# Kernel tuning notes

Hardware: AMD Instinct MI355X
Metric: run time of the kernel (lower is better)

## Reference

```python
import jax, jax.numpy as jnp
from jax import lax
import numpy as np

B, S, IN, H, L = 32, 512, 512, 1024, 4


def setup_inputs() -> dict:
    key = jax.random.key(0)
    ks = jax.random.split(key, 6)
    scale = 0.02
    return {
        "x": jax.random.normal(ks[0], (B, S, IN), jnp.float32),
        "w_ih0": jax.random.normal(ks[1], (3 * H, IN), jnp.float32) * scale,
        "w_hh0": jax.random.normal(ks[2], (3 * H, H), jnp.float32) * scale,
        "b0": jnp.zeros((3 * H,), jnp.float32),
        "w_ih_rest": jax.random.normal(ks[3], (L - 1, 3 * H, H), jnp.float32) * scale,
        "w_hh_rest": jax.random.normal(ks[4], (L - 1, 3 * H, H), jnp.float32) * scale,
        "b_rest": jnp.zeros((L - 1, 3 * H), jnp.float32),
    }


def _run_layer(xs, w_ih, w_hh, b):
    # xs: [B, S, D_in] -> outputs [B, S, H], final (h, c) each [B, H]
    batch = xs.shape[0]
    hid = w_hh.shape[1]

    def step(carry, x_t):
        h, c = carry
        gates = x_t @ w_ih.T + h @ w_hh.T + b  # [B, 3H]
        i_g, g_g, o_g = jnp.split(gates, 3, axis=1)
        c_next = c + jax.nn.sigmoid(i_g) * jnp.tanh(g_g)  # no forget gate (CEC)
        h_next = jax.nn.sigmoid(o_g) * jnp.tanh(c_next)
        return (h_next, c_next), h_next

    init = (jnp.zeros((batch, hid), xs.dtype), jnp.zeros((batch, hid), xs.dtype))
    (h_f, c_f), ys = lax.scan(step, init, jnp.swapaxes(xs, 0, 1))  # scan over time
    return jnp.swapaxes(ys, 0, 1), h_f, c_f


def reference(x, w_ih0, w_hh0, b0, w_ih_rest, w_hh_rest, b_rest):
    h_finals, c_finals = [], []
    cur, h_f, c_f = _run_layer(x, w_ih0, w_hh0, b0)
    h_finals.append(h_f)
    c_finals.append(c_f)
    for i in range(w_ih_rest.shape[0]):
        cur, h_f, c_f = _run_layer(cur, w_ih_rest[i], w_hh_rest[i], b_rest[i])
        h_finals.append(h_f)
        c_finals.append(c_f)
    return cur, (jnp.stack(h_finals), jnp.stack(c_finals))
```

## Files before the change

### kernel.cpp

```cpp
#include <hip/hip_runtime.h>


typedef unsigned short ushort_t;
typedef __attribute__((ext_vector_type(4))) float f32x4;
typedef __attribute__((ext_vector_type(8))) short s16x8;
typedef __attribute__((ext_vector_type(4))) short s16x4;

__device__ __forceinline__ unsigned short f2bf(float f) {
  union { float f; unsigned u; } v; v.f = f;
  unsigned r = (v.u + 0x7fffu + ((v.u >> 16) & 1u)) >> 16;
  return (unsigned short)r;
}
__device__ __forceinline__ float bf2f(unsigned short h) {
  union { unsigned u; float f; } v; v.u = ((unsigned)h) << 16; return v.f;
}
__device__ __forceinline__ void split2(float x, short& hi, short& lo) {
  unsigned short h = f2bf(x);
  hi = (short)h;
  lo = (short)f2bf(x - bf2f(h));
}

#define BM 128
#define BN 128
#define BK 32
__global__ __launch_bounds__(256) void k_gemm_split(
    const float* __restrict__ A, const float* __restrict__ Bw,
    const float* __restrict__ bias, float* __restrict__ C,
    int M, int N, int K) {
  __shared__ short Ah[BM * BK], Al[BM * BK];
  __shared__ short Bh[BN * BK], Bl[BN * BK];
  const int tid = threadIdx.x;
  const int nbm = M / BM;
  const int bm = blockIdx.x % nbm;
  const int bn = blockIdx.x / nbm;
  const int lane = tid & 63;
  const int wave = tid >> 6;
  const int wm = (wave & 1) * 64;
  const int wn = (wave >> 1) * 64;
  const int q = lane >> 4;
  f32x4 acc[4][4] = {};
  const int nk = K / BK;
  for (int kt = 0; kt < nk; ++kt) {
    __syncthreads();
    const int kb = kt * BK;
#pragma unroll
    for (int i = 0; i < 4; ++i) {
      int idx = tid + i * 256;
      int row = idx >> 3, c4 = (idx & 7) * 4;
      f32x4 ta = *(const f32x4*)(A + (size_t)(bm * BM + row) * K + kb + c4);
      s16x4 h4, l4;
#pragma unroll
      for (int j = 0; j < 4; ++j) { short hh, ll; split2(ta[j], hh, ll); h4[j] = hh; l4[j] = ll; }
      *(s16x4*)&Ah[row * BK + c4] = h4;
      *(s16x4*)&Al[row * BK + c4] = l4;
      f32x4 tb = *(const f32x4*)(Bw + (size_t)(bn * BN + row) * K + kb + c4);
#pragma unroll
      for (int j = 0; j < 4; ++j) { short hh, ll; split2(tb[j], hh, ll); h4[j] = hh; l4[j] = ll; }
      *(s16x4*)&Bh[row * BK + c4] = h4;
      *(s16x4*)&Bl[row * BK + c4] = l4;
    }
    __syncthreads();
    s16x8 ah[4], al[4], bh[4], bl[4];
#pragma unroll
    for (int i = 0; i < 4; ++i) {
      int r = (wm + i * 16 + (lane & 15)) * BK + q * 8;
      ah[i] = *(const s16x8*)&Ah[r];
      al[i] = *(const s16x8*)&Al[r];
      int rb = (wn + i * 16 + (lane & 15)) * BK + q * 8;
      bh[i] = *(const s16x8*)&Bh[rb];
      bl[i] = *(const s16x8*)&Bl[rb];
    }
#pragma unroll
    for (int mi = 0; mi < 4; ++mi)
#pragma unroll
      for (int ni = 0; ni < 4; ++ni) {
        acc[mi][ni] = __builtin_amdgcn_mfma_f32_16x16x32_bf16(ah[mi], bh[ni], acc[mi][ni], 0, 0, 0);
        acc[mi][ni] = __builtin_amdgcn_mfma_f32_16x16x32_bf16(al[mi], bh[ni], acc[mi][ni], 0, 0, 0);
        acc[mi][ni] = __builtin_amdgcn_mfma_f32_16x16x32_bf16(ah[mi], bl[ni], acc[mi][ni], 0, 0, 0);
      }
  }
#pragma unroll
  for (int mi = 0; mi < 4; ++mi)
#pragma unroll
    for (int ni = 0; ni < 4; ++ni) {
      int col = bn * BN + wn + ni * 16 + (lane & 15);
      float bv = bias[col];
#pragma unroll
      for (int r = 0; r < 4; ++r) {
        int row = bm * BM + wm + mi * 16 + q * 4 + r;
        C[(size_t)row * N + col] = acc[mi][ni][r] + bv;
      }
    }
}

__global__ __launch_bounds__(128) void k_recurrent(
    const float* __restrict__ Xp,
    const float* __restrict__ Whh,
    unsigned* __restrict__ hbuf,
    float* __restrict__ yOut,
    float* __restrict__ hOut,
    float* __restrict__ cOut,
    int* __restrict__ bar)
{
  __shared__ short Wh[128 * 12 * 8];
  __shared__ short Wl[128 * 12 * 8];
  __shared__ float red[2][16][16];
  const int tid = threadIdx.x;
  const int lane = tid & 63;
  const int g = tid >> 6;
  const int bid = blockIdx.x;
  const int s = ((bid & 7) << 5) | (bid >> 3);
  const int u0 = s * 4;
  const int b0 = g * 16;

  for (int p = tid; p < 1536; p += 128) {
    int n = p >> 7, kq = p & 127;
    int row = (n < 4) ? (u0 + n) : (n < 8) ? (1024 + u0 + (n - 4)) : (2048 + u0 + (n - 8));
    const float* src = Whh + (size_t)row * 1024 + kq * 8;
    f32x4 v0 = *(const f32x4*)src;
    f32x4 v1 = *(const f32x4*)(src + 4);
    s16x4 h4, l4;
#pragma unroll
    for (int j = 0; j < 4; ++j) { short hh, ll; split2(v0[j], hh, ll); h4[j] = hh; l4[j] = ll; }
    *(s16x4*)&Wh[(kq * 12 + n) * 8] = h4;
    *(s16x4*)&Wl[(kq * 12 + n) * 8] = l4;
#pragma unroll
    for (int j = 0; j < 4; ++j) { short hh, ll; split2(v1[j], hh, ll); h4[j] = hh; l4[j] = ll; }
    *(s16x4*)&Wh[(kq * 12 + n) * 8 + 4] = h4;
    *(s16x4*)&Wl[(kq * 12 + n) * 8 + 4] = l4;
  }

  const int m = lane & 15;
  const int q = lane >> 4;
  const bool nvalid = m < 12;
  const int eb = (tid >> 2) & 15;
  const int eu = tid & 3;
  const int kc0 = s & 31;
  float c = 0.f;
  __syncthreads();

  for (int t = 0; t < 512; ++t) {
    const int par = t & 1;
    const size_t mrow = (size_t)(b0 + eb) * 512 + t;
    const float xi = Xp[mrow * 3072 + (u0 + eu)];
    const float xg = Xp[mrow * 3072 + 1024 + (u0 + eu)];
    const float xo = Xp[mrow * 3072 + 2048 + (u0 + eu)];

    const unsigned* hp = hbuf + (size_t)par * 32768 + (b0 + m);
    f32x4 a0 = {0.f, 0.f, 0.f, 0.f}, a1 = a0, a2 = a0;
#pragma unroll 16
    for (int kci = 0; kci < 32; ++kci) {
      const int kc = (kci + kc0) & 31;
      const unsigned* p = hp + (kc * 32 + q * 8) * 32;
      unsigned w0 = __hip_atomic_load(p + 0 * 32, __ATOMIC_RELAXED, __HIP_MEMORY_SCOPE_AGENT);
      unsigned w1 = __hip_atomic_load(p + 1 * 32, __ATOMIC_RELAXED, __HIP_MEMORY_SCOPE_AGENT);
      unsigned w2 = __hip_atomic_load(p + 2 * 32, __ATOMIC_RELAXED, __HIP_MEMORY_SCOPE_AGENT);
      unsigned w3 = __hip_atomic_load(p + 3 * 32, __ATOMIC_RELAXED, __HIP_MEMORY_SCOPE_AGENT);
      unsigned w4 = __hip_atomic_load(p + 4 * 32, __ATOMIC_RELAXED, __HIP_MEMORY_SCOPE_AGENT);
      unsigned w5 = __hip_atomic_load(p + 5 * 32, __ATOMIC_RELAXED, __HIP_MEMORY_SCOPE_AGENT);
      unsigned w6 = __hip_atomic_load(p + 6 * 32, __ATOMIC_RELAXED, __HIP_MEMORY_SCOPE_AGENT);
      unsigned w7 = __hip_atomic_load(p + 7 * 32, __ATOMIC_RELAXED, __HIP_MEMORY_SCOPE_AGENT);
      union { unsigned u[4]; s16x8 v; } H, L;
      H.u[0] = (w0 >> 16) | (w1 & 0xffff0000u); L.u[0] = (w0 & 0xffffu) | (w1 << 16);
      H.u[1] = (w2 >> 16) | (w3 & 0xffff0000u); L.u[1] = (w2 & 0xffffu) | (w3 << 16);
      H.u[2] = (w4 >> 16) | (w5 & 0xffff0000u); L.u[2] = (w4 & 0xffffu) | (w5 << 16);
      H.u[3] = (w6 >> 16) | (w7 & 0xffff0000u); L.u[3] = (w6 & 0xffffu) | (w7 << 16);
      s16x8 ahf = H.v, alf = L.v;
      s16x8 bhf = {}, blf = {};
      if (nvalid) {
        bhf = *(const s16x8*)&Wh[(((kc * 4 + q) * 12) + m) * 8];
        blf = *(const s16x8*)&Wl[(((kc * 4 + q) * 12) + m) * 8];
      }
      a0 = __builtin_amdgcn_mfma_f32_16x16x32_bf16(ahf, bhf, a0, 0, 0, 0);
      a1 = __builtin_amdgcn_mfma_f32_16x16x32_bf16(alf, bhf, a1, 0, 0, 0);
      a2 = __builtin_amdgcn_mfma_f32_16x16x32_bf16(ahf, blf, a2, 0, 0, 0);
    }
#pragma unroll
    for (int r = 0; r < 4; ++r)
      red[g][q * 4 + r][m] = a0[r] + a1[r] + a2[r];
    __syncthreads();

    {
      float ig = xi + red[g][eb][eu];
      float gg = xg + red[g][eb][4 + eu];
      float og = xo + red[g][eb][8 + eu];
      float si = 1.f / (1.f + expf(-ig));
      float tg = tanhf(gg);
      c += si * tg;
      float so = 1.f / (1.f + expf(-og));
      float h = so * tanhf(c);
      short hh, hl;
      split2(h, hh, hl);
      unsigned hword = ((unsigned)(unsigned short)hh << 16) | (unsigned)(unsigned short)hl;
      size_t hw = (size_t)(1 - par) * 32768 + (size_t)(u0 + eu) * 32 + (b0 + eb);
      __hip_atomic_store(&hbuf[hw], hword, __ATOMIC_RELAXED, __HIP_MEMORY_SCOPE_AGENT);
      yOut[mrow * 1024 + (u0 + eu)] = h;
      if (t == 511) {
        hOut[(size_t)(b0 + eb) * 1024 + (u0 + eu)] = h;
        cOut[(size_t)(b0 + eb) * 1024 + (u0 + eu)] = c;
      }
    }
    if (t == 511) break;

    const int tgt = t + 1;
    asm volatile("s_waitcnt vmcnt(0)" ::: "memory");
    __syncthreads();
    if (bid == 0) {
      if (tid == 0)
        __hip_atomic_store(&bar[0], tgt, __ATOMIC_RELAXED, __HIP_MEMORY_SCOPE_AGENT);
      for (;;) {
        int f0 = __hip_atomic_load(&bar[tid], __ATOMIC_RELAXED, __HIP_MEMORY_SCOPE_AGENT);
        int f1 = __hip_atomic_load(&bar[tid + 128], __ATOMIC_RELAXED, __HIP_MEMORY_SCOPE_AGENT);
        if (__syncthreads_and((f0 >= tgt) && (f1 >= tgt))) break;
        __builtin_amdgcn_s_sleep(1);
      }
      if (tid == 0)
        __hip_atomic_store(&bar[256], tgt, __ATOMIC_RELAXED, __HIP_MEMORY_SCOPE_AGENT);
    } else {
      if (tid == 0) {
        __hip_atomic_store(&bar[bid], tgt, __ATOMIC_RELAXED, __HIP_MEMORY_SCOPE_AGENT);
        while (__hip_atomic_load(&bar[256], __ATOMIC_RELAXED, __HIP_MEMORY_SCOPE_AGENT) < tgt)
          __builtin_amdgcn_s_sleep(1);
      }
      __syncthreads();
    }
    asm volatile("" ::: "memory");
  }
}

extern "C" void kernel_launch(void* const* d_in, const int* in_sizes, int n_in,
                              void* d_out, int out_size, void* d_ws, size_t ws_size,
                              hipStream_t stream) {
  const float* x     = (const float*)d_in[0];
  const float* w_ih0 = (const float*)d_in[1];
  const float* w_hh0 = (const float*)d_in[2];
  const float* b0v   = (const float*)d_in[3];
  const float* w_ihr = (const float*)d_in[4];
  const float* w_hhr = (const float*)d_in[5];
  const float* b_r   = (const float*)d_in[6];
  float* out = (float*)d_out;

  char* ws = (char*)d_ws;
  float*    Xp   = (float*)(ws);
  unsigned* hbuf = (unsigned*)(ws + 201326592);
  int*      bar  = (int*)(ws + 201588736);

  float* yBuf     = out;
  float* hOutBase = out + 16777216;
  float* cOutBase = out + 16777216 + 131072;

  hipMemsetAsync(bar, 0, 8192, stream);

  for (int l = 0; l < 4; ++l) {
    const float* wih  = (l == 0) ? w_ih0 : (w_ihr + (size_t)(l - 1) * 3072 * 1024);
    const float* whh  = (l == 0) ? w_hh0 : (w_hhr + (size_t)(l - 1) * 3072 * 1024);
    const float* bias = (l == 0) ? b0v : (b_r + (size_t)(l - 1) * 3072);
    const int K = (l == 0) ? 512 : 1024;
    const float* Ain = (l == 0) ? x : yBuf;
    dim3 ggrid((16384 / BM) * (3072 / BN));
    k_gemm_split<<<ggrid, 256, 0, stream>>>(Ain, wih, bias, Xp, 16384, 3072, K);
    hipMemsetAsync(hbuf, 0, 262144, stream);
    float* hO = hOutBase + (size_t)l * 32768;
    float* cO = cOutBase + (size_t)l * 32768;
    int* barL = bar + l * 512;
    void* args[] = { (void*)&Xp, (void*)&whh, (void*)&hbuf, (void*)&yBuf,
                     (void*)&hO, (void*)&cO, (void*)&barL };
    if (hipLaunchCooperativeKernel((void*)k_recurrent, dim3(256), dim3(128),
                                   args, 0, stream) != hipSuccess) {
      k_recurrent<<<dim3(256), dim3(128), 0, stream>>>(Xp, whh, hbuf, yBuf,
                                                       hO, cO, barL);
    }
  }
}
```

Baseline: 19.13 ms.

## Remap recurrent blocks to one wave covering 8 units and 16 batches

The persistent recurrent kernel now uses a single 64-thread wave per block. Each block owns 8 hidden units (24 weight rows) for one 16-row batch group, where before a 128-thread block covered 4 units across two batch groups. Each wave issues twice as many MFMAs per h-fragment load, which halves the redundant hbuf reads per block and the per-unit LDS weight traffic. In exchange each block does twice the per-step serial MFMA work and the grid barrier handles four flags per thread.

```diff
diff --git a/kernel.cpp b/kernel.cpp
--- a/kernel.cpp
+++ b/kernel.cpp
@@ -93,7 +93,7 @@
     }
 }
 
-__global__ __launch_bounds__(128) void k_recurrent(
+__global__ __launch_bounds__(64) void k_recurrent(
     const float* __restrict__ Xp,
     const float* __restrict__ Whh,
     unsigned* __restrict__ hbuf,
@@ -102,53 +102,54 @@
     float* __restrict__ cOut,
     int* __restrict__ bar)
 {
-  __shared__ short Wh[128 * 12 * 8];
-  __shared__ short Wl[128 * 12 * 8];
-  __shared__ float red[2][16][16];
+  __shared__ short Wh[128 * 25 * 8];
+  __shared__ short Wl[128 * 25 * 8];
+  __shared__ float red[16][28];
   const int tid = threadIdx.x;
-  const int lane = tid & 63;
-  const int g = tid >> 6;
   const int bid = blockIdx.x;
-  const int s = ((bid & 7) << 5) | (bid >> 3);
-  const int u0 = s * 4;
-  const int b0 = g * 16;
-
-  for (int p = tid; p < 1536; p += 128) {
+  const int slice = ((bid & 7) << 4) | ((bid >> 3) & 15);
+  const int grp = bid >> 7;
+  const int u0 = slice * 8;
+  const int b0 = grp * 16;
+
+  for (int p = tid; p < 3072; p += 64) {
     int n = p >> 7, kq = p & 127;
-    int row = (n < 4) ? (u0 + n) : (n < 8) ? (1024 + u0 + (n - 4)) : (2048 + u0 + (n - 8));
+    int r = (n > 11) ? 1 : 0, rr = n - r * 12, G = rr >> 2, ui = rr & 3;
+    int row = G * 1024 + u0 + r * 4 + ui;
     const float* src = Whh + (size_t)row * 1024 + kq * 8;
     f32x4 v0 = *(const f32x4*)src;
     f32x4 v1 = *(const f32x4*)(src + 4);
     s16x4 h4, l4;
 #pragma unroll
     for (int j = 0; j < 4; ++j) { short hh, ll; split2(v0[j], hh, ll); h4[j] = hh; l4[j] = ll; }
-    *(s16x4*)&Wh[(kq * 12 + n) * 8] = h4;
-    *(s16x4*)&Wl[(kq * 12 + n) * 8] = l4;
+    *(s16x4*)&Wh[(kq * 25 + n) * 8] = h4;
+    *(s16x4*)&Wl[(kq * 25 + n) * 8] = l4;
 #pragma unroll
     for (int j = 0; j < 4; ++j) { short hh, ll; split2(v1[j], hh, ll); h4[j] = hh; l4[j] = ll; }
-    *(s16x4*)&Wh[(kq * 12 + n) * 8 + 4] = h4;
-    *(s16x4*)&Wl[(kq * 12 + n) * 8 + 4] = l4;
-  }
-
-  const int m = lane & 15;
-  const int q = lane >> 4;
+    *(s16x4*)&Wh[(kq * 25 + n) * 8 + 4] = h4;
+    *(s16x4*)&Wl[(kq * 25 + n) * 8 + 4] = l4;
+  }
+
+  const int m = tid & 15;
+  const int q = tid >> 4;
   const bool nvalid = m < 12;
-  const int eb = (tid >> 2) & 15;
-  const int eu = tid & 3;
-  const int kc0 = s & 31;
-  float c = 0.f;
+  const int kc0 = slice & 31;
+  float cA = 0.f, cB = 0.f;
   __syncthreads();
 
   for (int t = 0; t < 512; ++t) {
     const int par = t & 1;
-    const size_t mrow = (size_t)(b0 + eb) * 512 + t;
-    const float xi = Xp[mrow * 3072 + (u0 + eu)];
-    const float xg = Xp[mrow * 3072 + 1024 + (u0 + eu)];
-    const float xo = Xp[mrow * 3072 + 2048 + (u0 + eu)];
+    const size_t mrow = (size_t)(b0 + m) * 512 + t;
+    const float xiA = Xp[mrow * 3072 + (u0 + q)];
+    const float xiB = Xp[mrow * 3072 + (u0 + q + 4)];
+    const float xgA = Xp[mrow * 3072 + 1024 + (u0 + q)];
+    const float xgB = Xp[mrow * 3072 + 1024 + (u0 + q + 4)];
+    const float xoA = Xp[mrow * 3072 + 2048 + (u0 + q)];
+    const float xoB = Xp[mrow * 3072 + 2048 + (u0 + q + 4)];
 
     const unsigned* hp = hbuf + (size_t)par * 32768 + (b0 + m);
-    f32x4 a0 = {0.f, 0.f, 0.f, 0.f}, a1 = a0, a2 = a0;
-#pragma unroll 16
+    f32x4 acc[2][3] = {};
+#pragma unroll 8
     for (int kci = 0; kci < 32; ++kci) {
       const int kc = (kci + kc0) & 31;
       const unsigned* p = hp + (kc * 32 + q * 8) * 32;
@@ -166,38 +167,54 @@
       H.u[2] = (w4 >> 16) | (w5 & 0xffff0000u); L.u[2] = (w4 & 0xffffu) | (w5 << 16);
       H.u[3] = (w6 >> 16) | (w7 & 0xffff0000u); L.u[3] = (w6 & 0xffffu) | (w7 << 16);
       s16x8 ahf = H.v, alf = L.v;
-      s16x8 bhf = {}, blf = {};
-      if (nvalid) {
-        bhf = *(const s16x8*)&Wh[(((kc * 4 + q) * 12) + m) * 8];
-        blf = *(const s16x8*)&Wl[(((kc * 4 + q) * 12) + m) * 8];
-      }
-      a0 = __builtin_amdgcn_mfma_f32_16x16x32_bf16(ahf, bhf, a0, 0, 0, 0);
-      a1 = __builtin_amdgcn_mfma_f32_16x16x32_bf16(alf, bhf, a1, 0, 0, 0);
-      a2 = __builtin_amdgcn_mfma_f32_16x16x32_bf16(ahf, blf, a2, 0, 0, 0);
-    }
-#pragma unroll
-    for (int r = 0; r < 4; ++r)
-      red[g][q * 4 + r][m] = a0[r] + a1[r] + a2[r];
+#pragma unroll
+      for (int r = 0; r < 2; ++r) {
+        s16x8 bhf = {}, blf = {};
+        if (nvalid) {
+          bhf = *(const s16x8*)&Wh[(((kc * 4 + q) * 25) + r * 12 + m) * 8];
+          blf = *(const s16x8*)&Wl[(((kc * 4 + q) * 25) + r * 12 + m) * 8];
+        }
+        acc[r][0] = __builtin_amdgcn_mfma_f32_16x16x32_bf16(ahf, bhf, acc[r][0], 0, 0, 0);
+        acc[r][1] = __builtin_amdgcn_mfma_f32_16x16x32_bf16(alf, bhf, acc[r][1], 0, 0, 0);
+        acc[r][2] = __builtin_amdgcn_mfma_f32_16x16x32_bf16(ahf, blf, acc[r][2], 0, 0, 0);
+      }
+    }
+#pragma unroll
+    for (int r = 0; r < 2; ++r)
+#pragma unroll
+      for (int j = 0; j < 4; ++j)
+        red[q * 4 + j][r * 12 + m] = acc[r][0][j] + acc[r][1][j] + acc[r][2][j];
     __syncthreads();
 
     {
-      float ig = xi + red[g][eb][eu];
-      float gg = xg + red[g][eb][4 + eu];
-      float og = xo + red[g][eb][8 + eu];
-      float si = 1.f / (1.f + expf(-ig));
-      float tg = tanhf(gg);
-      c += si * tg;
-      float so = 1.f / (1.f + expf(-og));
-      float h = so * tanhf(c);
+      float igA = xiA + red[m][q];
+      float ggA = xgA + red[m][4 + q];
+      float ogA = xoA + red[m][8 + q];
+      float igB = xiB + red[m][12 + q];
+      float ggB = xgB + red[m][16 + q];
+      float ogB = xoB + red[m][20 + q];
+      float siA = 1.f / (1.f + expf(-igA));
+      cA += siA * tanhf(ggA);
+      float hA = (1.f / (1.f + expf(-ogA))) * tanhf(cA);
+      float siB = 1.f / (1.f + expf(-igB));
+      cB += siB * tanhf(ggB);
+      float hB = (1.f / (1.f + expf(-ogB))) * tanhf(cB);
       short hh, hl;
-      split2(h, hh, hl);
-      unsigned hword = ((unsigned)(unsigned short)hh << 16) | (unsigned)(unsigned short)hl;
-      size_t hw = (size_t)(1 - par) * 32768 + (size_t)(u0 + eu) * 32 + (b0 + eb);
-      __hip_atomic_store(&hbuf[hw], hword, __ATOMIC_RELAXED, __HIP_MEMORY_SCOPE_AGENT);
-      yOut[mrow * 1024 + (u0 + eu)] = h;
+      split2(hA, hh, hl);
+      unsigned wA = ((unsigned)(unsigned short)hh << 16) | (unsigned)(unsigned short)hl;
+      split2(hB, hh, hl);
+      unsigned wB = ((unsigned)(unsigned short)hh << 16) | (unsigned)(unsigned short)hl;
+      size_t hwA = (size_t)(1 - par) * 32768 + (size_t)(u0 + q) * 32 + (b0 + m);
+      size_t hwB = (size_t)(1 - par) * 32768 + (size_t)(u0 + q + 4) * 32 + (b0 + m);
+      __hip_atomic_store(&hbuf[hwA], wA, __ATOMIC_RELAXED, __HIP_MEMORY_SCOPE_AGENT);
+      __hip_atomic_store(&hbuf[hwB], wB, __ATOMIC_RELAXED, __HIP_MEMORY_SCOPE_AGENT);
+      yOut[mrow * 1024 + (u0 + q)] = hA;
+      yOut[mrow * 1024 + (u0 + q + 4)] = hB;
       if (t == 511) {
-        hOut[(size_t)(b0 + eb) * 1024 + (u0 + eu)] = h;
-        cOut[(size_t)(b0 + eb) * 1024 + (u0 + eu)] = c;
+        hOut[(size_t)(b0 + m) * 1024 + (u0 + q)] = hA;
+        hOut[(size_t)(b0 + m) * 1024 + (u0 + q + 4)] = hB;
+        cOut[(size_t)(b0 + m) * 1024 + (u0 + q)] = cA;
+        cOut[(size_t)(b0 + m) * 1024 + (u0 + q + 4)] = cB;
       }
     }
     if (t == 511) break;
@@ -210,8 +227,10 @@
         __hip_atomic_store(&bar[0], tgt, __ATOMIC_RELAXED, __HIP_MEMORY_SCOPE_AGENT);
       for (;;) {
         int f0 = __hip_atomic_load(&bar[tid], __ATOMIC_RELAXED, __HIP_MEMORY_SCOPE_AGENT);
-        int f1 = __hip_atomic_load(&bar[tid + 128], __ATOMIC_RELAXED, __HIP_MEMORY_SCOPE_AGENT);
-        if (__syncthreads_and((f0 >= tgt) && (f1 >= tgt))) break;
+        int f1 = __hip_atomic_load(&bar[tid + 64], __ATOMIC_RELAXED, __HIP_MEMORY_SCOPE_AGENT);
+        int f2 = __hip_atomic_load(&bar[tid + 128], __ATOMIC_RELAXED, __HIP_MEMORY_SCOPE_AGENT);
+        int f3 = __hip_atomic_load(&bar[tid + 192], __ATOMIC_RELAXED, __HIP_MEMORY_SCOPE_AGENT);
+        if (__syncthreads_and((f0 >= tgt) && (f1 >= tgt) && (f2 >= tgt) && (f3 >= tgt))) break;
         __builtin_amdgcn_s_sleep(1);
       }
       if (tid == 0)
@@ -265,10 +284,10 @@
     int* barL = bar + l * 512;
     void* args[] = { (void*)&Xp, (void*)&whh, (void*)&hbuf, (void*)&yBuf,
                      (void*)&hO, (void*)&cO, (void*)&barL };
-    if (hipLaunchCooperativeKernel((void*)k_recurrent, dim3(256), dim3(128),
+    if (hipLaunchCooperativeKernel((void*)k_recurrent, dim3(256), dim3(64),
                                    args, 0, stream) != hipSuccess) {
-      k_recurrent<<<dim3(256), dim3(128), 0, stream>>>(Xp, whh, hbuf, yBuf,
-                                                       hO, cO, barL);
-    }
-  }
-}
+      k_recurrent<<<dim3(256), dim3(64), 0, stream>>>(Xp, whh, hbuf, yBuf,
+                                                      hO, cO, barL);
+    }
+  }
+}
```

Measured after the change: 24.45 ms. 1.28x slower.
